# Optimization experiments

Measured on AMD Instinct MI355X. Metric: run time of the kernel, lower is better.

Reference implementation:

```python
import jax, jax.numpy as jnp
import numpy as np

N_HEAD = 16
ROPE_BASE = 10000.0


def _rope_cos_sin(T, D, dtype):
    # inv_freq over even dims, freqs concatenated twice (rotate_half convention)
    inv_freq = 1.0 / (ROPE_BASE ** (jnp.arange(0, D, 2, dtype=jnp.float32) / D))
    t = jnp.arange(T, dtype=jnp.float32)
    freqs = jnp.outer(t, inv_freq)          # [T, D/2]
    emb = jnp.concatenate([freqs, freqs], axis=-1)  # [T, D]
    return jnp.cos(emb).astype(dtype), jnp.sin(emb).astype(dtype)


def _rotate_half(x):
    x1, x2 = jnp.split(x, 2, axis=-1)
    return jnp.concatenate([-x2, x1], axis=-1)


def setup_inputs() -> dict:
    key = jax.random.key(0)
    ks = jax.random.split(key, 5)
    B, T, C = 2, 2048, 1024
    s = 1.0 / np.sqrt(C)
    return {
        "x": jax.random.normal(ks[0], (B, T, C), jnp.float32),
        "W_attn": jax.random.normal(ks[1], (C, 3 * C), jnp.float32) * s,
        "b_attn": jax.random.normal(ks[2], (3 * C,), jnp.float32) * 0.02,
        "W_proj": jax.random.normal(ks[3], (C, C), jnp.float32) * s,
        "b_proj": jax.random.normal(ks[4], (C,), jnp.float32) * 0.02,
    }


def reference(x, W_attn, b_attn, W_proj, b_proj):
    B, T, C = x.shape
    H = N_HEAD
    D = C // H

    # fused QKV projection
    qkv = x @ W_attn + b_attn                      # [B, T, 3C]
    q, k, v = jnp.split(qkv, 3, axis=-1)
    q = q.reshape(B, T, H, D).transpose(0, 2, 1, 3)  # [B, H, T, D]
    k = k.reshape(B, T, H, D).transpose(0, 2, 1, 3)
    v = v.reshape(B, T, H, D).transpose(0, 2, 1, 3)

    # RoPE (no past_kv: applied to full q and k)
    cos, sin = _rope_cos_sin(T, D, x.dtype)        # [T, D]
    cos = cos[None, None]                          # [1, 1, T, D]
    sin = sin[None, None]
    q = q * cos + _rotate_half(q) * sin
    k = k * cos + _rotate_half(k) * sin

    # causal SDPA (dropout_p = 0 in reference)
    scale = 1.0 / np.sqrt(D)
    scores = jnp.einsum("bhqd,bhkd->bhqk", q, k) * scale
    causal = jnp.tril(jnp.ones((T, T), dtype=bool))
    scores = jnp.where(causal, scores, jnp.finfo(scores.dtype).min)
    attn = jax.nn.softmax(scores, axis=-1)
    y = jnp.einsum("bhqk,bhkd->bhqd", attn, v)     # [B, H, T, D]

    y = y.transpose(0, 2, 1, 3).reshape(B, T, C)
    y = y @ W_proj + b_proj
    return y
```

## Files before the change

### kernel.cpp

```cpp
#include <hip/hip_runtime.h>
#include <cstdint>
#include <cstddef>

#define SEQ_T 2048
#define NHEAD 16

typedef __attribute__((ext_vector_type(8))) short short8;
typedef __attribute__((ext_vector_type(4))) float f32x4;
typedef __attribute__((ext_vector_type(16))) float f32x16;

__device__ __forceinline__ unsigned short f2bf(float f) {
  union { float f; unsigned int u; } v; v.f = f;
  return (unsigned short)((v.u + 0x7FFFu + ((v.u >> 16) & 1u)) >> 16);
}
__device__ __forceinline__ float bf2f(unsigned short u) {
  union { unsigned int u; float f; } v; v.u = ((unsigned int)u) << 16;
  return v.f;
}

#if __has_builtin(__builtin_amdgcn_exp2f)
__device__ __forceinline__ float hexp2(float x) { return __builtin_amdgcn_exp2f(x); }
#else
__device__ __forceinline__ float hexp2(float x) {
  float r;
  asm("v_exp_f32 %0, %1" : "=v"(r) : "v"(x));
  return r;
}
#endif

__device__ __forceinline__ unsigned cvtpk(float lo, float hi) {
  unsigned r;
  asm("v_cvt_pk_bf16_f32 %0, %1, %2" : "=v"(r) : "v"(lo), "v"(hi));
  return r;
}

__device__ __forceinline__ float max3f(float a, float b, float c) {
  float r;
  asm("v_max3_f32 %0, %1, %2, %3" : "=v"(r) : "v"(a), "v"(b), "v"(c));
  return r;
}

#if __has_builtin(__builtin_amdgcn_permlane32_swap)
__device__ __forceinline__ void plswap(unsigned& a, unsigned& b) {
  auto r = __builtin_amdgcn_permlane32_swap(a, b, false, false);
  a = r[0];
  b = r[1];
}
#else
__device__ __forceinline__ void plswap(unsigned& a, unsigned& b) {
  asm volatile("s_nop 1\n\tv_permlane32_swap_b32 %0, %1\n\ts_nop 1"
               : "+v"(a), "+v"(b));
}
#endif

__device__ __forceinline__ float xhalf_max(float x) {
  unsigned a = __builtin_bit_cast(unsigned, x), b = a;
  plswap(a, b);
  return fmaxf(__builtin_bit_cast(float, a), __builtin_bit_cast(float, b));
}
__device__ __forceinline__ float xhalf_add(float x) {
  unsigned a = __builtin_bit_cast(unsigned, x), b = a;
  plswap(a, b);
  return __builtin_bit_cast(float, a) + __builtin_bit_cast(float, b);
}

__device__ __forceinline__ float vmax16(const f32x16 v) {
  float m0 = max3f(v[0], v[1], v[2]);
  float m1 = max3f(v[3], v[4], v[5]);
  float m2 = max3f(v[6], v[7], v[8]);
  float m3 = max3f(v[9], v[10], v[11]);
  float m4 = max3f(v[12], v[13], v[14]);
  float m5 = max3f(m0, m1, v[15]);
  float m6 = max3f(m2, m3, m4);
  return fmaxf(m5, m6);
}

__device__ __forceinline__ void gl_lds16(const void* g, void* l) {
  __builtin_amdgcn_global_load_lds(
      (__attribute__((address_space(1))) void*)(void*)g,
      (__attribute__((address_space(3))) void*)l, 16, 0, 0);
}

__global__ void k_prep(const float* __restrict__ x,
                       const float* __restrict__ Wa,
                       const float* __restrict__ Wp,
                       unsigned short* __restrict__ xb,
                       unsigned short* __restrict__ wat,
                       unsigned short* __restrict__ wpt,
                       float2* __restrict__ tab) {
  const int b = blockIdx.x, tid = threadIdx.x;
  if (b < 4096) {
    int i = b * 256 + tid;
    float4 v = ((const float4*)x)[i];
    unsigned long long pk = (unsigned long long)f2bf(v.x)
                          | ((unsigned long long)f2bf(v.y) << 16)
                          | ((unsigned long long)f2bf(v.z) << 32)
                          | ((unsigned long long)f2bf(v.w) << 48);
    ((unsigned long long*)xb)[i] = pk;
  } else if (b < 5632) {
    int idx = (b - 4096) * 256 + tid;
    int n = idx % 3072, k0 = (idx / 3072) * 8;
    short8 v;
#pragma unroll
    for (int j = 0; j < 8; ++j)
      v[j] = (short)f2bf(Wa[(size_t)(k0 + j) * 3072 + n]);
    *(short8*)&wat[(size_t)n * 1024 + k0] = v;
  } else if (b < 6144) {
    int idx = (b - 5632) * 256 + tid;
    int n = idx & 1023, k0 = (idx >> 10) * 8;
    short8 v;
#pragma unroll
    for (int j = 0; j < 8; ++j)
      v[j] = (short)f2bf(Wp[(size_t)(k0 + j) * 1024 + n]);
    *(short8*)&wpt[(size_t)n * 1024 + k0] = v;
  } else {
    int idx = (b - 6144) * 256 + tid;
    int t = idx >> 5, i = idx & 31;
    float inv = powf(10000.0f, -(float)(2 * i) / 64.0f);
    float f = (float)t * inv;
    tab[idx] = make_float2(cosf(f), sinf(f));
  }
}

__global__ void k_gemm_qkv(const unsigned short* __restrict__ A,
                           const unsigned short* __restrict__ Bt,
                           const float* __restrict__ bias,
                           const float2* __restrict__ cs,
                           unsigned short* __restrict__ qo,
                           unsigned short* __restrict__ ko,
                           unsigned short* __restrict__ vo) {
  __shared__ unsigned short lA[128 * 32];
  __shared__ unsigned short lB[128 * 32];
  const int K = 1024;
  const int bn = blockIdx.x, bm = blockIdx.y;
  const int tid = threadIdx.x, w = tid >> 6, l = tid & 63;
  const int lr = l & 15, lh = l >> 4;
  const int wm = w >> 1, wn = w & 1;

  f32x4 acc[4][4];
#pragma unroll
  for (int m = 0; m < 4; ++m)
#pragma unroll
    for (int n = 0; n < 4; ++n)
#pragma unroll
      for (int i = 0; i < 4; ++i) acc[m][n][i] = 0.f;

  const unsigned short* ga0 = A + (size_t)(bm * 128 + w * 16 + (l >> 2)) * K + (l & 3) * 8;
  const unsigned short* gb0 = Bt + (size_t)(bn * 128 + w * 16 + (l >> 2)) * K + (l & 3) * 8;
  unsigned short* la0 = &lA[w * 512];
  unsigned short* la1 = &lA[(w + 4) * 512];
  unsigned short* lb0 = &lB[w * 512];
  unsigned short* lb1 = &lB[(w + 4) * 512];

  for (int kt = 0; kt < K; kt += 32) {
    gl_lds16(ga0 + kt, la0);
    gl_lds16(ga0 + (size_t)64 * K + kt, la1);
    gl_lds16(gb0 + kt, lb0);
    gl_lds16(gb0 + (size_t)64 * K + kt, lb1);
    __syncthreads();
    short8 af[4], bf[4];
#pragma unroll
    for (int m = 0; m < 4; ++m) af[m] = *(const short8*)&lA[(wm * 64 + m * 16 + lr) * 32 + lh * 8];
#pragma unroll
    for (int n = 0; n < 4; ++n) bf[n] = *(const short8*)&lB[(wn * 64 + n * 16 + lr) * 32 + lh * 8];
#pragma unroll
    for (int m = 0; m < 4; ++m)
#pragma unroll
      for (int n = 0; n < 4; ++n)
        acc[m][n] = __builtin_amdgcn_mfma_f32_16x16x32_bf16(af[m], bf[n], acc[m][n], 0, 0, 0);
    __syncthreads();
  }

  const int col0 = bn * 128 + wn * 64;
  const int row0 = bm * 128 + wm * 64;
  const int sec = col0 >> 10;
  const int hh = (col0 >> 6) & 15;
  float bl[4];
#pragma unroll
  for (int n = 0; n < 4; ++n) bl[n] = bias[col0 + n * 16 + lr];

  if (sec == 2) {
    const int b = row0 >> 11;
    unsigned short* vtp = vo + (size_t)(b * 16 + hh) * 64 * 2048;
#pragma unroll
    for (int n = 0; n < 4; ++n) {
      int d = n * 16 + lr;
#pragma unroll
      for (int m = 0; m < 4; ++m) {
        int t = (row0 + m * 16 + lh * 4) & 2047;
        unsigned long long pk = (unsigned long long)f2bf(acc[m][n][0] + bl[n])
                              | ((unsigned long long)f2bf(acc[m][n][1] + bl[n]) << 16)
                              | ((unsigned long long)f2bf(acc[m][n][2] + bl[n]) << 32)
                              | ((unsigned long long)f2bf(acc[m][n][3] + bl[n]) << 48);
        *(unsigned long long*)&vtp[(size_t)d * 2048 + t] = pk;
      }
    }
  } else {
    unsigned short* dst = (sec == 0) ? qo : ko;
#pragma unroll
    for (int m = 0; m < 4; ++m)
#pragma unroll
      for (int i = 0; i < 4; ++i) {
        int row = row0 + m * 16 + lh * 4 + i;
        int t = row & 2047, b = row >> 11;
        size_t ob = ((size_t)(b * 16 + hh) * 2048 + t) * 64;
#pragma unroll
        for (int n = 0; n < 4; ++n) {
          float v = acc[m][n][i] + bl[n];
          float pv = acc[m][n ^ 2][i] + bl[n ^ 2];
          int d = n * 16 + lr;
          float2 c = cs[t * 32 + (d & 31)];
          float rot = (d < 32) ? -pv : pv;
          dst[ob + d] = f2bf(v * c.x + rot * c.y);
        }
      }
  }
}

__global__ __launch_bounds__(512, 4) void k_attn(const unsigned short* __restrict__ Q,
                       const unsigned short* __restrict__ Kg,
                       const unsigned short* __restrict__ VT,
                       unsigned short* __restrict__ P0,
                       unsigned short* __restrict__ P1,
                       float2* __restrict__ ML) {
  __shared__ unsigned short smem[16896];
  const int id = blockIdx.x;
  const int xcd = id & 7, u = id >> 3;
  const int a = u & 31, sweep = u >> 5;
  const int g = a & 3, j = a >> 2;
  const int bh = xcd * 4 + g;
  const int qt = (sweep & 1) ? (15 - j) : j;
  const int sp = sweep >> 1;
  const int tid = threadIdx.x, w = tid >> 6, l = tid & 63;
  const int wq = w & 3, wk = w >> 2;
  const int lq = l & 31, hi = l >> 5;
  const size_t base = (size_t)bh * SEQ_T * 64;
  const float CE = 0.18033688f;
  const float DTHR = 44.3614f;

  const int qrow = qt * 128 + wq * 32 + lq;
  short8 qf[4];
#pragma unroll
  for (int c = 0; c < 4; ++c)
    qf[c] = *(const short8*)&Q[base + (size_t)qrow * 64 + c * 16 + hi * 8];

  const int r0 = tid >> 3, c8 = tid & 7;
  const unsigned short* ks0 = Kg + base + (size_t)r0 * 64 + ((c8 ^ (r0 & 7)) * 8);
  const unsigned short* vs0 = VT + base + (size_t)r0 * 2048 + ((c8 ^ (r0 & 7)) * 8);

#define STAGE(KT, B) do { \
    gl_lds16(ks0 + (size_t)(KT) * 4096, &smem[(B) * 4096 + w * 512]); \
    gl_lds16(vs0 + (size_t)(KT) * 64,   &smem[8192 + (B) * 4096 + w * 512]); \
  } while (0)

  float mi = -1.0e30f, li = 0.f;
  f32x16 oc0, oc1;
#pragma unroll
  for (int r = 0; r < 16; ++r) { oc0[r] = 0.f; oc1[r] = 0.f; }

  const int nit = qt + 1;
  const int kt0 = sp * nit;
  const int mfrom = 2 * qt;
  STAGE(kt0, 0);
  __syncthreads();

  for (int it = 0; it < nit; ++it) {
    const int cur = it & 1;
    const int kt = kt0 + it;
    if (it + 1 < nit) STAGE(kt + 1, cur ^ 1);
    const unsigned short* kb = &smem[cur * 4096];
    const unsigned short* vb = &smem[8192 + cur * 4096];

    f32x16 st;
#pragma unroll
    for (int r = 0; r < 16; ++r) st[r] = 0.f;
    __builtin_amdgcn_s_setprio(1);
#pragma unroll
    for (int c = 0; c < 4; ++c) {
      const short8 kf = *(const short8*)&kb[(wk * 32 + lq) * 64 + (((2 * c + hi) ^ (lq & 7)) * 8)];
      st = __builtin_amdgcn_mfma_f32_32x32x16_bf16(kf, qf[c], st, 0, 0, 0);
    }
    __builtin_amdgcn_s_setprio(0);

    if (kt >= mfrom) {
#pragma unroll
      for (int r = 0; r < 16; ++r) {
        int kvg = kt * 64 + wk * 32 + (r & 3) + 8 * (r >> 2) + 4 * hi;
        if (kvg > qrow) st[r] = -3.0e38f;
      }
    }

    float tm = xhalf_max(vmax16(st));
    if (!__all(tm <= mi + DTHR)) {
      float mn = fmaxf(mi, tm);
      float scq = hexp2((mi - mn) * CE);
      mi = mn;
      li *= scq;
#pragma unroll
      for (int r = 0; r < 16; ++r) {
        float sc_r = __shfl(scq, (r & 3) + 8 * (r >> 2) + 4 * hi, 64);
        oc0[r] *= sc_r;
        oc1[r] *= sc_r;
      }
    }
    const float nb = mi * CE;
    float rs = 0.f;
#pragma unroll
    for (int r = 0; r < 16; ++r) {
      float p = hexp2(fmaf(st[r], CE, -nb));
      st[r] = p;
      rs += p;
    }
    li += rs;

    short8 pa[2];
#pragma unroll
    for (int kc = 0; kc < 2; ++kc) {
      const int o = kc * 8;
      unsigned w0 = cvtpk(st[o + 0], st[o + 1]);
      unsigned w1 = cvtpk(st[o + 2], st[o + 3]);
      unsigned w2 = cvtpk(st[o + 4], st[o + 5]);
      unsigned w3 = cvtpk(st[o + 6], st[o + 7]);
      plswap(w0, w2);
      plswap(w1, w3);
      uint4 F;
      F.x = w0; F.y = w1; F.z = w2; F.w = w3;
      pa[kc] = __builtin_bit_cast(short8, F);
    }

    {
      short8 vbf[2][2];
#pragma unroll
      for (int dt = 0; dt < 2; ++dt)
#pragma unroll
        for (int kc = 0; kc < 2; ++kc)
          vbf[dt][kc] = *(const short8*)&vb[(dt * 32 + lq) * 64 +
                          (((wk * 4 + kc * 2 + hi) ^ (lq & 7)) * 8)];
      __builtin_amdgcn_s_setprio(1);
#pragma unroll
      for (int kc = 0; kc < 2; ++kc) {
        oc0 = __builtin_amdgcn_mfma_f32_32x32x16_bf16(pa[kc], vbf[0][kc], oc0, 0, 0, 0);
        oc1 = __builtin_amdgcn_mfma_f32_32x32x16_bf16(pa[kc], vbf[1][kc], oc1, 0, 0, 0);
      }
      __builtin_amdgcn_s_setprio(0);
    }

    if (it + 1 < nit) __syncthreads();
  }

  li = xhalf_add(li);

  __syncthreads();
  float* obuf = (float*)smem;
  float* mlb  = (float*)&smem[16384];
  if (wk == 1) {
#pragma unroll
    for (int r = 0; r < 16; ++r) {
      const int q = (r & 3) + 8 * (r >> 2) + 4 * hi;
      obuf[wq * 2048 + q * 64 + lq]      = oc0[r];
      obuf[wq * 2048 + q * 64 + 32 + lq] = oc1[r];
    }
    if (hi == 0) {
      mlb[wq * 64 + lq * 2 + 0] = mi;
      mlb[wq * 64 + lq * 2 + 1] = li;
    }
  }
  __syncthreads();
  if (wk == 0) {
    unsigned short* dst = sp ? P1 : P0;
    const int hh = bh & 15, bb = bh >> 4;
#pragma unroll
    for (int r = 0; r < 16; ++r) {
      const int q = (r & 3) + 8 * (r >> 2) + 4 * hi;
      float m0 = __shfl(mi, q, 64), l0 = __shfl(li, q, 64);
      float m1 = mlb[wq * 64 + q * 2 + 0], l1 = mlb[wq * 64 + q * 2 + 1];
      float mm = fmaxf(m0, m1);
      float f0 = hexp2((m0 - mm) * CE), f1 = hexp2((m1 - mm) * CE);
      float dn = f0 * l0 + f1 * l1;
      float inv = (dn > 0.f) ? (1.0f / dn) : 0.f;
      float o0 = (f0 * oc0[r] + f1 * obuf[wq * 2048 + q * 64 + lq]) * inv;
      float o1 = (f0 * oc1[r] + f1 * obuf[wq * 2048 + q * 64 + 32 + lq]) * inv;
      int qg = qt * 128 + wq * 32 + q;
      size_t ob = (size_t)(bb * 2048 + qg) * 1024 + hh * 64;
      dst[ob + lq]      = f2bf(o0);
      dst[ob + 32 + lq] = f2bf(o1);
      if (lq == 0) ML[(size_t)(sp * 32 + bh) * 2048 + qg] = make_float2(mm, dn);
    }
  }
#undef STAGE
}

__global__ void k_combine(const unsigned short* __restrict__ P1,
                          const float2* __restrict__ ML,
                          unsigned short* __restrict__ P0) {
  const float CE = 0.18033688f;
  int idx = blockIdx.x * 256 + threadIdx.x;
  int flat = idx * 8;
  int c = flat & 1023, t = (flat >> 10) & 2047, b = flat >> 21;
  int bh = b * 16 + (c >> 6);
  float2 a0 = ML[(size_t)bh * 2048 + t];
  float2 a1 = ML[(size_t)(32 + bh) * 2048 + t];
  float mm = fmaxf(a0.x, a1.x);
  float w0 = hexp2((a0.x - mm) * CE) * a0.y;
  float w1 = hexp2((a1.x - mm) * CE) * a1.y;
  float inv = 1.0f / (w0 + w1);
  w0 *= inv; w1 *= inv;
  short8 o0 = *(const short8*)&P0[flat];
  short8 o1 = *(const short8*)&P1[flat];
  short8 o;
#pragma unroll
  for (int k = 0; k < 8; ++k)
    o[k] = (short)f2bf(w0 * bf2f((unsigned short)o0[k]) + w1 * bf2f((unsigned short)o1[k]));
  *(short8*)&P0[flat] = o;
}

__global__ void k_gemm_proj(const unsigned short* __restrict__ A,
                            const unsigned short* __restrict__ Bt,
                            const float* __restrict__ bias,
                            float* __restrict__ out) {
  __shared__ unsigned short lA[64 * 32];
  __shared__ unsigned short lB[128 * 32];
  const int K = 1024;
  const int bn = blockIdx.x, bm = blockIdx.y;
  const int tid = threadIdx.x, w = tid >> 6, l = tid & 63;
  const int lr = l & 15, lh = l >> 4;
  const int wm = w >> 1, wn = w & 1;

  f32x4 acc[2][4];
#pragma unroll
  for (int m = 0; m < 2; ++m)
#pragma unroll
    for (int n = 0; n < 4; ++n)
#pragma unroll
      for (int i = 0; i < 4; ++i) acc[m][n][i] = 0.f;

  const unsigned short* ga0 = A + (size_t)(bm * 64 + (tid >> 2)) * K + (tid & 3) * 8;
  const unsigned short* gb0 = Bt + (size_t)(bn * 128 + w * 16 + (l >> 2)) * K + (l & 3) * 8;
  unsigned short* la0 = &lA[w * 512];
  unsigned short* lb0 = &lB[w * 512];
  unsigned short* lb1 = &lB[(w + 4) * 512];

  for (int kt = 0; kt < K; kt += 32) {
    gl_lds16(ga0 + kt, la0);
    gl_lds16(gb0 + kt, lb0);
    gl_lds16(gb0 + (size_t)64 * K + kt, lb1);
    __syncthreads();
    short8 af[2], bf[4];
#pragma unroll
    for (int m = 0; m < 2; ++m) af[m] = *(const short8*)&lA[(wm * 32 + m * 16 + lr) * 32 + lh * 8];
#pragma unroll
    for (int n = 0; n < 4; ++n) bf[n] = *(const short8*)&lB[(wn * 64 + n * 16 + lr) * 32 + lh * 8];
#pragma unroll
    for (int m = 0; m < 2; ++m)
#pragma unroll
      for (int n = 0; n < 4; ++n)
        acc[m][n] = __builtin_amdgcn_mfma_f32_16x16x32_bf16(af[m], bf[n], acc[m][n], 0, 0, 0);
    __syncthreads();
  }

  const int col0 = bn * 128 + wn * 64;
  const int row0 = bm * 64 + wm * 32;
  float bl[4];
#pragma unroll
  for (int n = 0; n < 4; ++n) bl[n] = bias[col0 + n * 16 + lr];
#pragma unroll
  for (int m = 0; m < 2; ++m)
#pragma unroll
    for (int i = 0; i < 4; ++i) {
      int row = row0 + m * 16 + lh * 4 + i;
#pragma unroll
      for (int n = 0; n < 4; ++n)
        out[(size_t)row * 1024 + col0 + n * 16 + lr] = acc[m][n][i] + bl[n];
    }
}

extern "C" void kernel_launch(void* const* d_in, const int* in_sizes, int n_in,
                              void* d_out, int out_size, void* d_ws, size_t ws_size,
                              hipStream_t stream) {
  const float* x     = (const float*)d_in[0];
  const float* Wattn = (const float*)d_in[1];
  const float* battn = (const float*)d_in[2];
  const float* Wproj = (const float*)d_in[3];
  const float* bproj = (const float*)d_in[4];
  float* out = (float*)d_out;

  char* ws = (char*)d_ws;
  unsigned short* xb  = (unsigned short*)(ws);
  unsigned short* wat = (unsigned short*)(ws + (8ull  << 20));
  unsigned short* wpt = (unsigned short*)(ws + (14ull << 20));
  unsigned short* qa  = (unsigned short*)(ws + (16ull << 20));
  unsigned short* ka  = (unsigned short*)(ws + (24ull << 20));
  unsigned short* va  = (unsigned short*)(ws + (32ull << 20));
  unsigned short* ob  = (unsigned short*)(ws + (40ull << 20));
  float2* cs          = (float2*)(ws + (48ull << 20));
  float2* ml          = (float2*)wat;

  k_prep<<<6400, 256, 0, stream>>>(x, Wattn, Wproj, xb, wat, wpt, cs);
  k_gemm_qkv<<<dim3(24, 32), 256, 0, stream>>>(xb, wat, battn, cs, qa, ka, va);
  k_attn<<<1024, 512, 0, stream>>>(qa, ka, va, ob, xb, ml);
  k_combine<<<2048, 256, 0, stream>>>(xb, ml, ob);
  k_gemm_proj<<<dim3(8, 64), 256, 0, stream>>>(ob, wpt, bproj, out);
}
```

Measured before the change: 117.0 us.

## Double GEMM K-tile to 64 and XOR-swizzle LDS layout in QKV/proj GEMMs

Both the QKV and output-projection GEMMs now stage 64-wide K tiles per iteration instead of 32. This halves the number of barrier pairs and loop iterations. The global-to-LDS load mapping is changed to 8 threads per row, with an XOR swizzle on the 16-byte column chunk keyed on the row. MFMA fragment reads apply the same swizzle, which is meant to avoid LDS bank conflicts under the wider row stride. LDS use per block doubles, which may reduce occupancy.

```diff
diff --git a/kernel.cpp b/kernel.cpp
--- a/kernel.cpp
+++ b/kernel.cpp
@@ -129,8 +129,8 @@
                            unsigned short* __restrict__ qo,
                            unsigned short* __restrict__ ko,
                            unsigned short* __restrict__ vo) {
-  __shared__ unsigned short lA[128 * 32];
-  __shared__ unsigned short lB[128 * 32];
+  __shared__ unsigned short lA[128 * 64];
+  __shared__ unsigned short lB[128 * 64];
   const int K = 1024;
   const int bn = blockIdx.x, bm = blockIdx.y;
   const int tid = threadIdx.x, w = tid >> 6, l = tid & 63;
@@ -145,29 +145,39 @@
 #pragma unroll
       for (int i = 0; i < 4; ++i) acc[m][n][i] = 0.f;
 
-  const unsigned short* ga0 = A + (size_t)(bm * 128 + w * 16 + (l >> 2)) * K + (l & 3) * 8;
-  const unsigned short* gb0 = Bt + (size_t)(bn * 128 + w * 16 + (l >> 2)) * K + (l & 3) * 8;
-  unsigned short* la0 = &lA[w * 512];
-  unsigned short* la1 = &lA[(w + 4) * 512];
-  unsigned short* lb0 = &lB[w * 512];
-  unsigned short* lb1 = &lB[(w + 4) * 512];
-
-  for (int kt = 0; kt < K; kt += 32) {
-    gl_lds16(ga0 + kt, la0);
-    gl_lds16(ga0 + (size_t)64 * K + kt, la1);
-    gl_lds16(gb0 + kt, lb0);
-    gl_lds16(gb0 + (size_t)64 * K + kt, lb1);
+  const int srow = tid >> 3;
+  const int scol = ((tid & 7) ^ (srow & 7)) * 8;
+  const unsigned short* ga0 = A + (size_t)(bm * 128 + srow) * K + scol;
+  const unsigned short* gb0 = Bt + (size_t)(bn * 128 + srow) * K + scol;
+  unsigned short* lad = &lA[w * 512];
+  unsigned short* lbd = &lB[w * 512];
+
+  for (int kt = 0; kt < K; kt += 64) {
+#pragma unroll
+    for (int rep = 0; rep < 4; ++rep) {
+      gl_lds16(ga0 + (size_t)rep * 32 * K + kt, lad + rep * 2048);
+      gl_lds16(gb0 + (size_t)rep * 32 * K + kt, lbd + rep * 2048);
+    }
     __syncthreads();
-    short8 af[4], bf[4];
-#pragma unroll
-    for (int m = 0; m < 4; ++m) af[m] = *(const short8*)&lA[(wm * 64 + m * 16 + lr) * 32 + lh * 8];
-#pragma unroll
-    for (int n = 0; n < 4; ++n) bf[n] = *(const short8*)&lB[(wn * 64 + n * 16 + lr) * 32 + lh * 8];
-#pragma unroll
-    for (int m = 0; m < 4; ++m)
-#pragma unroll
-      for (int n = 0; n < 4; ++n)
-        acc[m][n] = __builtin_amdgcn_mfma_f32_16x16x32_bf16(af[m], bf[n], acc[m][n], 0, 0, 0);
+#pragma unroll
+    for (int ks = 0; ks < 2; ++ks) {
+      short8 af[4], bf[4];
+#pragma unroll
+      for (int m = 0; m < 4; ++m) {
+        const int row = wm * 64 + m * 16 + lr;
+        af[m] = *(const short8*)&lA[row * 64 + (((ks * 4 + lh) ^ (row & 7)) * 8)];
+      }
+#pragma unroll
+      for (int n = 0; n < 4; ++n) {
+        const int row = wn * 64 + n * 16 + lr;
+        bf[n] = *(const short8*)&lB[row * 64 + (((ks * 4 + lh) ^ (row & 7)) * 8)];
+      }
+#pragma unroll
+      for (int m = 0; m < 4; ++m)
+#pragma unroll
+        for (int n = 0; n < 4; ++n)
+          acc[m][n] = __builtin_amdgcn_mfma_f32_16x16x32_bf16(af[m], bf[n], acc[m][n], 0, 0, 0);
+    }
     __syncthreads();
   }
 
@@ -418,8 +428,8 @@
                             const unsigned short* __restrict__ Bt,
                             const float* __restrict__ bias,
                             float* __restrict__ out) {
-  __shared__ unsigned short lA[64 * 32];
-  __shared__ unsigned short lB[128 * 32];
+  __shared__ unsigned short lA[64 * 64];
+  __shared__ unsigned short lB[128 * 64];
   const int K = 1024;
   const int bn = blockIdx.x, bm = blockIdx.y;
   const int tid = threadIdx.x, w = tid >> 6, l = tid & 63;
@@ -434,27 +444,40 @@
 #pragma unroll
       for (int i = 0; i < 4; ++i) acc[m][n][i] = 0.f;
 
-  const unsigned short* ga0 = A + (size_t)(bm * 64 + (tid >> 2)) * K + (tid & 3) * 8;
-  const unsigned short* gb0 = Bt + (size_t)(bn * 128 + w * 16 + (l >> 2)) * K + (l & 3) * 8;
-  unsigned short* la0 = &lA[w * 512];
-  unsigned short* lb0 = &lB[w * 512];
-  unsigned short* lb1 = &lB[(w + 4) * 512];
-
-  for (int kt = 0; kt < K; kt += 32) {
-    gl_lds16(ga0 + kt, la0);
-    gl_lds16(gb0 + kt, lb0);
-    gl_lds16(gb0 + (size_t)64 * K + kt, lb1);
+  const int srow = tid >> 3;
+  const int scol = ((tid & 7) ^ (srow & 7)) * 8;
+  const unsigned short* ga0 = A + (size_t)(bm * 64 + srow) * K + scol;
+  const unsigned short* gb0 = Bt + (size_t)(bn * 128 + srow) * K + scol;
+  unsigned short* lad = &lA[w * 512];
+  unsigned short* lbd = &lB[w * 512];
+
+  for (int kt = 0; kt < K; kt += 64) {
+#pragma unroll
+    for (int rep = 0; rep < 2; ++rep)
+      gl_lds16(ga0 + (size_t)rep * 32 * K + kt, lad + rep * 2048);
+#pragma unroll
+    for (int rep = 0; rep < 4; ++rep)
+      gl_lds16(gb0 + (size_t)rep * 32 * K + kt, lbd + rep * 2048);
     __syncthreads();
-    short8 af[2], bf[4];
-#pragma unroll
-    for (int m = 0; m < 2; ++m) af[m] = *(const short8*)&lA[(wm * 32 + m * 16 + lr) * 32 + lh * 8];
-#pragma unroll
-    for (int n = 0; n < 4; ++n) bf[n] = *(const short8*)&lB[(wn * 64 + n * 16 + lr) * 32 + lh * 8];
-#pragma unroll
-    for (int m = 0; m < 2; ++m)
-#pragma unroll
-      for (int n = 0; n < 4; ++n)
-        acc[m][n] = __builtin_amdgcn_mfma_f32_16x16x32_bf16(af[m], bf[n], acc[m][n], 0, 0, 0);
+#pragma unroll
+    for (int ks = 0; ks < 2; ++ks) {
+      short8 af[2], bf[4];
+#pragma unroll
+      for (int m = 0; m < 2; ++m) {
+        const int row = wm * 32 + m * 16 + lr;
+        af[m] = *(const short8*)&lA[row * 64 + (((ks * 4 + lh) ^ (row & 7)) * 8)];
+      }
+#pragma unroll
+      for (int n = 0; n < 4; ++n) {
+        const int row = wn * 64 + n * 16 + lr;
+        bf[n] = *(const short8*)&lB[row * 64 + (((ks * 4 + lh) ^ (row & 7)) * 8)];
+      }
+#pragma unroll
+      for (int m = 0; m < 2; ++m)
+#pragma unroll
+        for (int n = 0; n < 4; ++n)
+          acc[m][n] = __builtin_amdgcn_mfma_f32_16x16x32_bf16(af[m], bf[n], acc[m][n], 0, 0, 0);
+    }
     __syncthreads();
   }
 
```

Result: no change. 114.9 us (-1.8%).
